# Performance work log

Measured on AMD Instinct MI355X. Metric: run time of the kernel, lower is better.

## Reference

```python
import jax, jax.numpy as jnp
import numpy as np

EPS = 1e-5  # torch BatchNorm1d default

def setup_inputs() -> dict:
    B, I, O, F = 32, 512, 720, 321
    key = jax.random.key(0)
    k = jax.random.split(key, 7)
    x = jax.random.normal(k[0], (B, I, F), dtype=jnp.float32)
    # per-timestep Linear weights stacked: W[f] is the f-th nn.Linear (out, in)
    bound = 1.0 / np.sqrt(I)
    W = jax.random.uniform(k[1], (F, O, I), dtype=jnp.float32, minval=-bound, maxval=bound)
    b = jax.random.uniform(k[2], (F, O), dtype=jnp.float32, minval=-bound, maxval=bound)
    # BatchNorm1d(num_feats) affine params + running stats (eval-mode semantics)
    gamma = jnp.ones((F,), dtype=jnp.float32)
    beta = jnp.zeros((F,), dtype=jnp.float32)
    running_mean = jax.random.normal(k[3], (F,), dtype=jnp.float32) * 0.1
    running_var = jax.random.uniform(k[4], (F,), dtype=jnp.float32, minval=0.5, maxval=1.5)
    return {"x": x, "W": W, "b": b, "gamma": gamma, "beta": beta,
            "running_mean": running_mean, "running_var": running_var}

def reference(x, W, b, gamma, beta, running_mean, running_var):
    # x: [B, I, F]. BatchNorm1d over the feature (F) channel, applied elementwise
    # over batch and in_channels (permute/permute in torch is just a broadcast here).
    inv = gamma * jax.lax.rsqrt(running_var + EPS)          # [F]
    xn = x * inv + (beta - running_mean * inv)              # [B, I, F]
    # 321 independent Linears fused into one batched GEMM:
    # out[b, o, f] = sum_i xn[b, i, f] * W[f, o, i] + b[f, o]
    out = jnp.einsum('bif,foi->bof', xn, W) + b.T[None]     # [B, O, F]
    return out
```

## Files before the change

### kernel.cpp

```cpp
#include <hip/hip_runtime.h>
#include <stdint.h>

#define F_DIM 321
#define O_DIM 720
#define I_DIM 512
#define B_DIM 32
#define G_F 8

typedef __attribute__((ext_vector_type(8))) short short8;
typedef __attribute__((ext_vector_type(4))) float f32x4;
typedef __attribute__((ext_vector_type(4))) uint32_t u32x4;
typedef __attribute__((ext_vector_type(2))) uint32_t u32x2;

__device__ __forceinline__ uint32_t rne_pack2(float lo, float hi) {
  uint32_t a = __builtin_bit_cast(uint32_t, lo);
  uint32_t b = __builtin_bit_cast(uint32_t, hi);
  a += 0x7FFFu + ((a >> 16) & 1u);
  b += 0x7FFFu + ((b >> 16) & 1u);
  return (a >> 16) | (b & 0xFFFF0000u);
}

__global__ void __launch_bounds__(256) xn_pack_kernel(
    const float* __restrict__ x, const float* __restrict__ gamma,
    const float* __restrict__ beta, const float* __restrict__ rmean,
    const float* __restrict__ rvar, u32x4* __restrict__ ws) {
  __shared__ float tile[8 * F_DIM];
  const int iblk = blockIdx.x;
  const int b    = blockIdx.y;
  const float* src = x + ((size_t)b * I_DIM + (size_t)iblk * 8) * F_DIM;
  for (int idx = threadIdx.x; idx < 8 * F_DIM; idx += 256)
    tile[idx] = src[idx];
  __syncthreads();
  for (int f = threadIdx.x; f < F_DIM; f += 256) {
    float inv = gamma[f] * rsqrtf(rvar[f] + 1e-5f);
    float sh  = beta[f] - rmean[f] * inv;
    float v[8];
#pragma unroll
    for (int j = 0; j < 8; ++j) v[j] = fmaf(tile[j * F_DIM + f], inv, sh);
    u32x4 pk;
    pk.x = rne_pack2(v[0], v[1]);
    pk.y = rne_pack2(v[2], v[3]);
    pk.z = rne_pack2(v[4], v[5]);
    pk.w = rne_pack2(v[6], v[7]);
    ws[(size_t)f * 2048 + iblk * 32 + b] = pk;
  }
}

__global__ void __launch_bounds__(256) linear_bn_kernel(
    const float* __restrict__ Wt, const float* __restrict__ bias,
    const u32x4* __restrict__ xn, float* __restrict__ out) {
  __shared__ u32x4 lds4[2048];
  char* ldsb = (char*)lds4;
  const int tid  = threadIdx.x;
  const int lane = tid & 63;
  const int wv   = tid >> 6;
  const int quad = lane >> 4;
  const int t16  = lane & 15;
  const int mtile = wv & 1;
  const int ntile = wv >> 1;

  const int d   = blockIdx.y * 23 + blockIdx.x;
  const int xcd = d & 7, idx = d >> 3;
  const int w   = (xcd < 7) ? xcd * 118 + idx : 826 + idx;
  const int bx  = w % 23;
  const int by  = w / 23;

  const int o0 = bx * 32;
  const int fb = by * G_F;
  const int nf = min(G_F, F_DIM - fb);
  const int oC = o0 + ntile * 16 + t16;

  const int sc  = tid & 127;
  const int shi = tid >> 7;

  f32x4 acc[G_F];
#pragma unroll
  for (int ff = 0; ff < G_F; ++ff) {
    float bv = 0.0f;
    if (ff < nf && oC < O_DIM) bv = bias[(size_t)(fb + ff) * O_DIM + oC];
    acc[ff] = (f32x4){bv, bv, bv, bv};
  }

  u32x2 pk[16];
  auto stage_load = [&](int f) {
    const float* fbase = Wt + (size_t)f * (O_DIM * I_DIM) + sc * 4;
#pragma unroll
    for (int j = 0; j < 16; ++j) {
      const int row = min(o0 + 2 * j + shi, O_DIM - 1);
      f32x4 a = *(const f32x4*)(fbase + (size_t)row * I_DIM);
      u32x2 p;
      p.x = rne_pack2(a.x, a.y);
      p.y = rne_pack2(a.z, a.w);
      pk[j] = p;
    }
  };

  stage_load(fb);
#pragma unroll
  for (int ff = 0; ff < G_F; ++ff) {
    if (ff >= nf) break;
    __syncthreads();
#pragma unroll
    for (int j = 0; j < 16; ++j) {
      const int o = 2 * j + shi;
      const int byte = ((o * 128 + sc) * 8) ^ ((o & 7) << 4);
      *(u32x2*)(ldsb + byte) = pk[j];
    }
    __syncthreads();
    if (ff + 1 < nf) stage_load(fb + ff + 1);
    const int f = fb + ff;
    const u32x4* xf = xn + (size_t)f * 2048 + mtile * 16 + t16;
    const int orow = ntile * 16 + t16;
    const int swz  = (t16 & 7) << 4;
#pragma unroll
    for (int kk = 0; kk < 16; ++kk) {
      u32x4 av = xf[(kk * 4 + quad) * 32];
      u32x4 bv = *(const u32x4*)(
          ldsb + ((orow * 1024 + kk * 64 + quad * 16) ^ swz));
      acc[ff] = __builtin_amdgcn_mfma_f32_16x16x32_bf16(
          __builtin_bit_cast(short8, av), __builtin_bit_cast(short8, bv),
          acc[ff], 0, 0, 0);
    }
  }

  if (oC < O_DIM) {
#pragma unroll
    for (int r = 0; r < 4; ++r) {
      const int brow = mtile * 16 + quad * 4 + r;
      float* po = out + ((size_t)brow * O_DIM + oC) * F_DIM + fb;
#pragma unroll
      for (int ff = 0; ff < G_F; ++ff)
        if (ff < nf) po[ff] = acc[ff][r];
    }
  }
}

extern "C" void kernel_launch(void* const* d_in, const int* in_sizes, int n_in,
                              void* d_out, int out_size, void* d_ws, size_t ws_size,
                              hipStream_t stream) {
  const float* x     = (const float*)d_in[0];
  const float* W     = (const float*)d_in[1];
  const float* b     = (const float*)d_in[2];
  const float* gamma = (const float*)d_in[3];
  const float* beta  = (const float*)d_in[4];
  const float* rmean = (const float*)d_in[5];
  const float* rvar  = (const float*)d_in[6];
  u32x4* ws = (u32x4*)d_ws;

  xn_pack_kernel<<<dim3(64, 32), 256, 0, stream>>>(x, gamma, beta, rmean, rvar, ws);
  linear_bn_kernel<<<dim3(23, 41), 256, 0, stream>>>(W, b, ws, (float*)d_out);
}
```

Baseline: 679.3 us.

## Stage fp32 weights via direct global-to-LDS loads and convert after LDS reads

Weight tiles are now copied straight from global memory into LDS as fp32 with global_load_lds, with a swizzle, instead of being loaded into registers, packed to bf16 and written to LDS. The bf16 conversion moves to the consumer side after reading LDS, and the activation fragments are prefetched into registers before the barrier. This cuts register staging and VGPR pressure, and launch_bounds now requests 2 blocks per CU. In exchange, LDS use doubles to 64KB, the load of the next weight tile no longer overlaps with the MFMA work, and each weight element gets redundant conversion work per wave.

```diff
diff --git a/kernel.cpp b/kernel.cpp
--- a/kernel.cpp
+++ b/kernel.cpp
@@ -10,7 +10,6 @@
 typedef __attribute__((ext_vector_type(8))) short short8;
 typedef __attribute__((ext_vector_type(4))) float f32x4;
 typedef __attribute__((ext_vector_type(4))) uint32_t u32x4;
-typedef __attribute__((ext_vector_type(2))) uint32_t u32x2;
 
 __device__ __forceinline__ uint32_t rne_pack2(float lo, float hi) {
   uint32_t a = __builtin_bit_cast(uint32_t, lo);
@@ -18,6 +17,12 @@
   a += 0x7FFFu + ((a >> 16) & 1u);
   b += 0x7FFFu + ((b >> 16) & 1u);
   return (a >> 16) | (b & 0xFFFF0000u);
+}
+
+__device__ __forceinline__ void gload_lds16(const void* g, void* l) {
+  __builtin_amdgcn_global_load_lds(
+      (const __attribute__((address_space(1))) uint32_t*)g,
+      (__attribute__((address_space(3))) uint32_t*)l, 16, 0, 0);
 }
 
 __global__ void __launch_bounds__(256) xn_pack_kernel(
@@ -46,10 +51,10 @@
   }
 }
 
-__global__ void __launch_bounds__(256) linear_bn_kernel(
+__global__ void __launch_bounds__(256, 2) linear_bn_kernel(
     const float* __restrict__ Wt, const float* __restrict__ bias,
     const u32x4* __restrict__ xn, float* __restrict__ out) {
-  __shared__ u32x4 lds4[2048];
+  __shared__ u32x4 lds4[4096];
   char* ldsb = (char*)lds4;
   const int tid  = threadIdx.x;
   const int lane = tid & 63;
@@ -70,9 +75,6 @@
   const int nf = min(G_F, F_DIM - fb);
   const int oC = o0 + ntile * 16 + t16;
 
-  const int sc  = tid & 127;
-  const int shi = tid >> 7;
-
   f32x4 acc[G_F];
 #pragma unroll
   for (int ff = 0; ff < G_F; ++ff) {
@@ -81,44 +83,45 @@
     acc[ff] = (f32x4){bv, bv, bv, bv};
   }
 
-  u32x2 pk[16];
-  auto stage_load = [&](int f) {
-    const float* fbase = Wt + (size_t)f * (O_DIM * I_DIM) + sc * 4;
+  auto stage = [&](int f) {
+    const char* fbase = (const char*)Wt + (size_t)f * (O_DIM * I_DIM * 4);
 #pragma unroll
     for (int j = 0; j < 16; ++j) {
-      const int row = min(o0 + 2 * j + shi, O_DIM - 1);
-      f32x4 a = *(const f32x4*)(fbase + (size_t)row * I_DIM);
-      u32x2 p;
-      p.x = rne_pack2(a.x, a.y);
-      p.y = rne_pack2(a.z, a.w);
-      pk[j] = p;
+      const int k = wv * 16 + j;
+      const int o = min(o0 + (k >> 1), O_DIM - 1);
+      const int s = ((k >> 1) & 7) << 4;
+      const char* g = fbase + (size_t)o * 2048 + (k & 1) * 1024
+                      + ((16 * lane) ^ s);
+      gload_lds16(g, ldsb + k * 1024);
     }
   };
 
-  stage_load(fb);
+  const int orow = ntile * 16 + t16;
+  const int swz  = (t16 & 7) << 4;
+
 #pragma unroll
   for (int ff = 0; ff < G_F; ++ff) {
     if (ff >= nf) break;
+    if (ff) __syncthreads();
+    stage(fb + ff);
+    const int f = fb + ff;
+    const u32x4* xf = xn + (size_t)f * 2048 + mtile * 16 + t16;
+    u32x4 av[16];
+#pragma unroll
+    for (int kk = 0; kk < 16; ++kk) av[kk] = xf[(kk * 4 + quad) * 32];
     __syncthreads();
 #pragma unroll
-    for (int j = 0; j < 16; ++j) {
-      const int o = 2 * j + shi;
-      const int byte = ((o * 128 + sc) * 8) ^ ((o & 7) << 4);
-      *(u32x2*)(ldsb + byte) = pk[j];
-    }
-    __syncthreads();
-    if (ff + 1 < nf) stage_load(fb + ff + 1);
-    const int f = fb + ff;
-    const u32x4* xf = xn + (size_t)f * 2048 + mtile * 16 + t16;
-    const int orow = ntile * 16 + t16;
-    const int swz  = (t16 & 7) << 4;
-#pragma unroll
     for (int kk = 0; kk < 16; ++kk) {
-      u32x4 av = xf[(kk * 4 + quad) * 32];
-      u32x4 bv = *(const u32x4*)(
-          ldsb + ((orow * 1024 + kk * 64 + quad * 16) ^ swz));
+      const int lin = orow * 2048 + kk * 128 + quad * 32;
+      f32x4 w0 = *(const f32x4*)(ldsb + ((lin) ^ swz));
+      f32x4 w1 = *(const f32x4*)(ldsb + ((lin + 16) ^ swz));
+      u32x4 bv;
+      bv.x = rne_pack2(w0.x, w0.y);
+      bv.y = rne_pack2(w0.z, w0.w);
+      bv.z = rne_pack2(w1.x, w1.y);
+      bv.w = rne_pack2(w1.z, w1.w);
       acc[ff] = __builtin_amdgcn_mfma_f32_16x16x32_bf16(
-          __builtin_bit_cast(short8, av), __builtin_bit_cast(short8, bv),
+          __builtin_bit_cast(short8, av[kk]), __builtin_bit_cast(short8, bv),
           acc[ff], 0, 0, 0);
     }
   }
```

Result: no change. 672.9 us (-0.9%).
